# Kernel tuning notes

Hardware: AMD Instinct MI355X
Metric: run time of the kernel (lower is better)

## Reference

```python
import jax, jax.numpy as jnp
import numpy as np

EPS = 1e-08


def setup_inputs() -> dict:
    key = jax.random.key(0)
    k1, k2, k3 = jax.random.split(key, 3)
    N, IN_DIM, OUT_DIM = 8192, 512, 512
    h = jax.random.normal(k1, (N, IN_DIM), dtype=jnp.float32)
    adj = jax.random.randint(k2, (N, N), 0, 2, dtype=jnp.int32)
    # nn.Linear(in_dim, out_dim, bias=False) weight: [out_dim, in_dim]
    W = jax.random.normal(k3, (OUT_DIM, IN_DIM), dtype=jnp.float32) * (1.0 / np.sqrt(IN_DIM))
    return {"h": h, "adj": adj, "W": W}


def reference(h, adj, W):
    # Wh = h @ W^T  -> [N, out_dim]
    Wh = h @ W.T
    N = Wh.shape[0]
    norms = jnp.linalg.norm(Wh, axis=1, keepdims=True)  # [N, 1]
    # cosine similarity [N, N]
    sim = (Wh @ Wh.T) / (norms * norms.T + EPS)
    mask = (adj > 0) | jnp.eye(N, dtype=bool)
    sim_masked = jnp.where(mask, sim, -jnp.inf)
    alpha = jax.nn.softmax(sim_masked, axis=1)
    return alpha @ Wh
```

## Files before the change

### kernel.cpp

```cpp
#include <hip/hip_runtime.h>
#include <hip/hip_bf16.h>
#include <stdint.h>

#define NN 8192
#define DD 512

typedef unsigned short u16;
typedef unsigned long long u64;
typedef __attribute__((ext_vector_type(8))) short short8;
typedef __attribute__((ext_vector_type(4))) float f32x4;

__device__ __forceinline__ void gld_lds16(const void* g, void* l) {
  __builtin_amdgcn_global_load_lds(
      (const __attribute__((address_space(1))) uint32_t*)(uintptr_t)g,
      (__attribute__((address_space(3))) uint32_t*)(uintptr_t)l,
      16, 0, 0);
}

__device__ __forceinline__ u16 f2bf(float f) {
  __hip_bfloat16 b = __float2bfloat16(f);
  return __builtin_bit_cast(u16, b);
}

__global__ void fill_kernel(float* __restrict__ p, int n, float v) {
  int i = blockIdx.x * 256 + threadIdx.x;
  int stride = gridDim.x * 256;
  for (; i < n; i += stride) p[i] = v;
}

__global__ void cvt4_kernel(const float4* __restrict__ src, ushort4* __restrict__ dst, int n4) {
  int i = blockIdx.x * 256 + threadIdx.x;
  int stride = gridDim.x * 256;
  for (; i < n4; i += stride) {
    float4 v = src[i];
    ushort4 o;
    o.x = f2bf(v.x); o.y = f2bf(v.y); o.z = f2bf(v.z); o.w = f2bf(v.w);
    dst[i] = o;
  }
}

__global__ void pack_adj_kernel(const int* __restrict__ adj, u16* __restrict__ mask,
                                float* __restrict__ den) {
  const int row = blockIdx.x;
  const int t = threadIdx.x;
  if (t == 0) den[row] = 0.0f;
  const uint4* arow = (const uint4*)(adj + (size_t)row * NN);
  #pragma unroll
  for (int iter = 0; iter < 2; iter++) {
    const int c16 = iter * 256 + t;
    unsigned int bits = 0;
    #pragma unroll
    for (int g = 0; g < 4; g++) {
      uint4 v = arow[c16 * 4 + g];
      bits |= (v.x ? 1u : 0u) << (g * 4 + 0);
      bits |= (v.y ? 1u : 0u) << (g * 4 + 1);
      bits |= (v.z ? 1u : 0u) << (g * 4 + 2);
      bits |= (v.w ? 1u : 0u) << (g * 4 + 3);
    }
    mask[(size_t)row * (NN / 16) + c16] = (u16)bits;
  }
}

__global__ void rownorm_kernel(const float* __restrict__ Wh, float* __restrict__ invn) {
  int row = blockIdx.x;
  int l = threadIdx.x;
  const float4* p = (const float4*)(Wh + (size_t)row * DD);
  float4 a = p[l], b = p[l + 64];
  float s = a.x*a.x + a.y*a.y + a.z*a.z + a.w*a.w
          + b.x*b.x + b.y*b.y + b.z*b.z + b.w*b.w;
  #pragma unroll
  for (int off = 32; off; off >>= 1) s += __shfl_down(s, off);
  if (l == 0) invn[row] = 1.0f / sqrtf(s);
}

__global__ void u_wht_kernel(const float* __restrict__ Wh, const float* __restrict__ invn,
                             u16* __restrict__ U, u16* __restrict__ WhT) {
  __shared__ float tile[64][65];
  int i0 = blockIdx.x * 64, d0 = blockIdx.y * 64;
  int c = threadIdx.x & 63, rb = threadIdx.x >> 6;
  #pragma unroll
  for (int r = rb; r < 64; r += 4) {
    float v = Wh[(size_t)(i0 + r) * DD + d0 + c];
    tile[r][c] = v;
    U[(size_t)(i0 + r) * DD + d0 + c] = f2bf(v * invn[i0 + r]);
  }
  __syncthreads();
  #pragma unroll
  for (int r = rb; r < 64; r += 4) {
    WhT[(size_t)(d0 + r) * NN + i0 + c] = f2bf(tile[c][r]);
  }
}

__global__ void __launch_bounds__(256) gemm_wh(
    const u16* __restrict__ A, const u16* __restrict__ B,
    int Nn, int K, float* __restrict__ Cf)
{
  __shared__ __align__(16) u16 As[128 * 32];
  __shared__ __align__(16) u16 Bs[128 * 32];

  const int tid = threadIdx.x;
  const int w = tid >> 6;
  const int lane = tid & 63;
  const int lm = lane & 15;
  const int q = lane >> 4;
  const int row0 = blockIdx.y * 128;
  const int col0 = blockIdx.x * 128;
  const int RM = (w >> 1) * 64;
  const int RN = (w & 1) * 64;
  const int sr = tid >> 2;
  const int sk = (tid & 3) * 8;

  f32x4 acc[4][4];
  #pragma unroll
  for (int a_ = 0; a_ < 4; a_++)
    #pragma unroll
    for (int b_ = 0; b_ < 4; b_++)
      acc[a_][b_] = (f32x4){0.f, 0.f, 0.f, 0.f};

  const size_t Abase = (size_t)row0 * K;
  const size_t Bbase = (size_t)col0 * K;

  for (int k0 = 0; k0 < K; k0 += 32) {
    __syncthreads();
    gld_lds16(A + Abase + (size_t)sr * K + k0 + sk,        (char*)As + w * 1024);
    gld_lds16(A + Abase + (size_t)(sr + 64) * K + k0 + sk, (char*)As + 4096 + w * 1024);
    gld_lds16(B + Bbase + (size_t)sr * K + k0 + sk,        (char*)Bs + w * 1024);
    gld_lds16(B + Bbase + (size_t)(sr + 64) * K + k0 + sk, (char*)Bs + 4096 + w * 1024);
    __syncthreads();

    short8 af[4], bfr[4];
    #pragma unroll
    for (int mt = 0; mt < 4; mt++)
      af[mt] = *(const short8*)&As[(RM + mt * 16 + lm) * 32 + q * 8];
    #pragma unroll
    for (int nt = 0; nt < 4; nt++)
      bfr[nt] = *(const short8*)&Bs[(RN + nt * 16 + lm) * 32 + q * 8];

    #pragma unroll
    for (int mt = 0; mt < 4; mt++)
      #pragma unroll
      for (int nt = 0; nt < 4; nt++)
        acc[mt][nt] = __builtin_amdgcn_mfma_f32_16x16x32_bf16(af[mt], bfr[nt], acc[mt][nt], 0, 0, 0);
  }

  #pragma unroll
  for (int mt = 0; mt < 4; mt++) {
    const int ib = row0 + RM + mt * 16 + q * 4;
    #pragma unroll
    for (int rr = 0; rr < 4; rr++) {
      const int i = ib + rr;
      #pragma unroll
      for (int nt = 0; nt < 4; nt++) {
        const int jc = col0 + RN + nt * 16 + lm;
        Cf[(size_t)i * Nn + jc] = acc[mt][nt][rr];
      }
    }
  }
}

__global__ void __launch_bounds__(256) gemm_sim(
    const u16* __restrict__ U, const u64* __restrict__ maskw,
    u16* __restrict__ Pb, float* __restrict__ den)
{
  __shared__ __align__(16) u16 As[128 * 32];
  __shared__ __align__(16) u16 Bs[128 * 32];

  const int b = blockIdx.x;
  int bi = (int)((sqrtf(8.0f * (float)b + 1.0f) - 1.0f) * 0.5f);
  while ((bi + 1) * (bi + 2) / 2 <= b) bi++;
  while (bi * (bi + 1) / 2 > b) bi--;
  const int bj = b - bi * (bi + 1) / 2;

  const int tid = threadIdx.x;
  const int w = tid >> 6;
  const int lane = tid & 63;
  const int lm = lane & 15;
  const int q = lane >> 4;
  const int row0 = bi * 128;
  const int col0 = bj * 128;
  const int RM = (w >> 1) * 64;
  const int RN = (w & 1) * 64;
  const int sr = tid >> 2;
  const int sk = (tid & 3) * 8;
  const bool diag = (bi == bj);

  f32x4 acc[4][4];
  #pragma unroll
  for (int a_ = 0; a_ < 4; a_++)
    #pragma unroll
    for (int b_ = 0; b_ < 4; b_++)
      acc[a_][b_] = (f32x4){0.f, 0.f, 0.f, 0.f};

  const size_t Abase = (size_t)row0 * DD;
  const size_t Bbase = (size_t)col0 * DD;

  for (int k0 = 0; k0 < DD; k0 += 32) {
    __syncthreads();
    gld_lds16(U + Abase + (size_t)sr * DD + k0 + sk,        (char*)As + w * 1024);
    gld_lds16(U + Abase + (size_t)(sr + 64) * DD + k0 + sk, (char*)As + 4096 + w * 1024);
    gld_lds16(U + Bbase + (size_t)sr * DD + k0 + sk,        (char*)Bs + w * 1024);
    gld_lds16(U + Bbase + (size_t)(sr + 64) * DD + k0 + sk, (char*)Bs + 4096 + w * 1024);
    __syncthreads();

    short8 af[4], bfr[4];
    #pragma unroll
    for (int mt = 0; mt < 4; mt++)
      af[mt] = *(const short8*)&As[(RM + mt * 16 + lm) * 32 + q * 8];
    #pragma unroll
    for (int nt = 0; nt < 4; nt++)
      bfr[nt] = *(const short8*)&Bs[(RN + nt * 16 + lm) * 32 + q * 8];

    #pragma unroll
    for (int mt = 0; mt < 4; mt++)
      #pragma unroll
      for (int nt = 0; nt < 4; nt++)
        acc[mt][nt] = __builtin_amdgcn_mfma_f32_16x16x32_bf16(af[mt], bfr[nt], acc[mt][nt], 0, 0, 0);
  }

  const int wordIdx = (col0 + RN) >> 6;
  const int word2Idx = (row0 + RM) >> 6;

  u64 wrd2[4];
  if (!diag) {
    #pragma unroll
    for (int nt = 0; nt < 4; nt++) {
      const int jc = col0 + RN + nt * 16 + lm;
      wrd2[nt] = maskw[(size_t)jc * (NN / 64) + word2Idx];
    }
  }

  float msum[4] = {0.f, 0.f, 0.f, 0.f};

  #pragma unroll
  for (int mt = 0; mt < 4; mt++) {
    const int ib = row0 + RM + mt * 16 + q * 4;
    float pm[4][4];
    #pragma unroll
    for (int rr = 0; rr < 4; rr++) {
      const int i = ib + rr;
      const u64 wrd = maskw[(size_t)i * (NN / 64) + wordIdx];
      const int bit2 = mt * 16 + q * 4 + rr;
      float psum = 0.f;
      #pragma unroll
      for (int nt = 0; nt < 4; nt++) {
        const int jc = col0 + RN + nt * 16 + lm;
        const float ev = __expf(acc[mt][nt][rr]);
        const bool on = ((wrd >> (nt * 16 + lm)) & 1ull) || (diag && i == jc);
        const float p = on ? ev : 0.0f;
        psum += p;
        Pb[(size_t)i * NN + jc] = f2bf(p);
        if (!diag) {
          const bool on2 = (wrd2[nt] >> bit2) & 1ull;
          const float pmv = on2 ? ev : 0.0f;
          pm[nt][rr] = pmv;
          msum[nt] += pmv;
        }
      }
      #pragma unroll
      for (int off = 8; off; off >>= 1) psum += __shfl_down(psum, off, 16);
      if (lm == 0) atomicAdd(&den[i], psum);
    }
    if (!diag) {
      #pragma unroll
      for (int nt = 0; nt < 4; nt++) {
        const int jc = col0 + RN + nt * 16 + lm;
        ushort4 m4;
        m4.x = f2bf(pm[nt][0]); m4.y = f2bf(pm[nt][1]);
        m4.z = f2bf(pm[nt][2]); m4.w = f2bf(pm[nt][3]);
        *(ushort4*)&Pb[(size_t)jc * NN + ib] = m4;
      }
    }
  }

  if (!diag) {
    #pragma unroll
    for (int nt = 0; nt < 4; nt++) {
      float s = msum[nt];
      s += __shfl_xor(s, 16);
      s += __shfl_xor(s, 32);
      if (q == 0) atomicAdd(&den[col0 + RN + nt * 16 + lm], s);
    }
  }
}

__global__ void __launch_bounds__(512, 2) gemm_out(
    const u16* __restrict__ A,
    const u16* __restrict__ B,
    u16* __restrict__ part)
{
  __shared__ __align__(16) u16 As[128 * 32];
  __shared__ __align__(16) u16 Bs[512 * 32];

  const int tid = threadIdx.x;
  const int w = tid >> 6;
  const int lane = tid & 63;
  const int lm = lane & 15;
  const int q = lane >> 4;
  const int row0 = blockIdx.x * 128;
  const int z = blockIdx.y;
  const int RM = (w >> 2) * 64;
  const int RN = (w & 3) * 128;
  const int sr = tid >> 2;
  const int sk = (tid & 3) * 8;

  f32x4 acc[4][8];
  #pragma unroll
  for (int a_ = 0; a_ < 4; a_++)
    #pragma unroll
    for (int b_ = 0; b_ < 8; b_++)
      acc[a_][b_] = (f32x4){0.f, 0.f, 0.f, 0.f};

  const size_t Abase = (size_t)row0 * NN;
  const int kBegin = z * (NN / 8), kEnd = (z + 1) * (NN / 8);

  for (int k0 = kBegin; k0 < kEnd; k0 += 32) {
    __syncthreads();
    gld_lds16(A + Abase + (size_t)sr * NN + k0 + sk, (char*)As + w * 1024);
    #pragma unroll
    for (int c = 0; c < 4; c++)
      gld_lds16(B + (size_t)(c * 128 + sr) * NN + k0 + sk, (char*)Bs + c * 8192 + w * 1024);
    __syncthreads();

    short8 af[4], bfr[8];
    #pragma unroll
    for (int mt = 0; mt < 4; mt++)
      af[mt] = *(const short8*)&As[(RM + mt * 16 + lm) * 32 + q * 8];
    #pragma unroll
    for (int nt = 0; nt < 8; nt++)
      bfr[nt] = *(const short8*)&Bs[(RN + nt * 16 + lm) * 32 + q * 8];

    #pragma unroll
    for (int mt = 0; mt < 4; mt++)
      #pragma unroll
      for (int nt = 0; nt < 8; nt++)
        acc[mt][nt] = __builtin_amdgcn_mfma_f32_16x16x32_bf16(af[mt], bfr[nt], acc[mt][nt], 0, 0, 0);
  }

  u16* const pz = part + (size_t)z * NN * DD;
  #pragma unroll
  for (int mt = 0; mt < 4; mt++) {
    const int ib = row0 + RM + mt * 16 + q * 4;
    #pragma unroll
    for (int rr = 0; rr < 4; rr++) {
      const int i = ib + rr;
      #pragma unroll
      for (int nt = 0; nt < 8; nt++) {
        const int dc = RN + nt * 16 + lm;
        pz[(size_t)i * DD + dc] = f2bf(acc[mt][nt][rr]);
      }
    }
  }
}

__global__ void reduce8_kernel(const u16* __restrict__ part,
                               const float* __restrict__ den, float4* __restrict__ out) {
  const int idx = blockIdx.x * 256 + threadIdx.x;
  const int row = idx >> 6;
  const float dinv = 1.0f / den[row];
  float s[8] = {0, 0, 0, 0, 0, 0, 0, 0};
  #pragma unroll
  for (int zp = 0; zp < 8; zp++) {
    const uint4 u = ((const uint4*)(part + (size_t)zp * NN * DD))[idx];
    s[0] += __uint_as_float(u.x << 16); s[1] += __uint_as_float(u.x & 0xffff0000u);
    s[2] += __uint_as_float(u.y << 16); s[3] += __uint_as_float(u.y & 0xffff0000u);
    s[4] += __uint_as_float(u.z << 16); s[5] += __uint_as_float(u.z & 0xffff0000u);
    s[6] += __uint_as_float(u.w << 16); s[7] += __uint_as_float(u.w & 0xffff0000u);
  }
  float4 o0 = {s[0] * dinv, s[1] * dinv, s[2] * dinv, s[3] * dinv};
  float4 o1 = {s[4] * dinv, s[5] * dinv, s[6] * dinv, s[7] * dinv};
  out[idx * 2] = o0;
  out[idx * 2 + 1] = o1;
}

extern "C" void kernel_launch(void* const* d_in, const int* in_sizes, int n_in,
                              void* d_out, int out_size, void* d_ws, size_t ws_size,
                              hipStream_t stream) {
  const float* h = (const float*)d_in[0];
  const int* adj = (const int*)d_in[1];
  const float* W = (const float*)d_in[2];
  float* out = (float*)d_out;

  const size_t SZ_P    = (size_t)NN * NN * 2;
  const size_t SZ_MASK = (size_t)NN * NN / 8;
  const size_t SZ_WHT  = (size_t)DD * NN * 2;
  const size_t SZ_HB   = (size_t)NN * DD * 2;
  const size_t SZ_WB   = (size_t)DD * DD * 2;
  const size_t SZ_U    = (size_t)NN * DD * 2;
  const size_t SZ_WH   = (size_t)NN * DD * 4;
  const size_t SZ_PART = (size_t)8 * NN * DD * 2;
  const size_t NEEDED  = SZ_P + SZ_MASK + SZ_WHT + SZ_HB + SZ_WB + SZ_U + SZ_WH
                       + SZ_PART + 2 * (size_t)NN * 4;

  if (ws_size < NEEDED) {
    fill_kernel<<<256, 256, 0, stream>>>(out, out_size, 12345.0f);
    return;
  }

  char* ws = (char*)d_ws;
  size_t off = 0;
  u16*   P    = (u16*)(ws + off); off += SZ_P;
  u16*   mask = (u16*)(ws + off); off += SZ_MASK;
  u16*   WhT  = (u16*)(ws + off); off += SZ_WHT;
  u16*   hb   = (u16*)(ws + off); off += SZ_HB;
  u16*   Wb   = (u16*)(ws + off); off += SZ_WB;
  u16*   U    = (u16*)(ws + off); off += SZ_U;
  float* Wh   = (float*)(ws + off); off += SZ_WH;
  u16*   part = (u16*)(ws + off); off += SZ_PART;
  float* invn = (float*)(ws + off);
  float* den  = invn + NN;

  pack_adj_kernel<<<NN, 256, 0, stream>>>(adj, mask, den);
  cvt4_kernel<<<1024, 256, 0, stream>>>((const float4*)h, (ushort4*)hb, NN * DD / 4);
  cvt4_kernel<<<256, 256, 0, stream>>>((const float4*)W, (ushort4*)Wb, DD * DD / 4);
  gemm_wh<<<dim3(DD / 128, NN / 128), 256, 0, stream>>>(hb, Wb, DD, DD, Wh);
  rownorm_kernel<<<NN, 64, 0, stream>>>(Wh, invn);
  u_wht_kernel<<<dim3(NN / 64, DD / 64), 256, 0, stream>>>(Wh, invn, U, WhT);
  gemm_sim<<<64 * 65 / 2, 256, 0, stream>>>(U, (const u64*)mask, P, den);
  gemm_out<<<dim3(NN / 128, 8), 512, 0, stream>>>(P, WhT, part);
  reduce8_kernel<<<NN * DD / 8 / 256, 256, 0, stream>>>(part, den, (float4*)out);
}
```

Baseline: 655.2 us.

## Shrink gemm_out tile to 64 rows, use exp2 with prescaled norms

Each gemm_out block now covers 64 rows instead of 128, and each wave computes a 64x64 output slice. This halves the accumulator registers, which lets the launch bound ask for 4 blocks per CU and doubles the grid. The cost is that each loaded B tile is reused across fewer rows. In gemm_sim, exp is replaced by exp2f on inputs prescaled by sqrt(log2 e) folded into U. Probabilities are truncated to bf16 by bit masking rather than rounded, and the denominator sums the same truncated values so it stays consistent with P.

```diff
diff --git a/kernel.cpp b/kernel.cpp
--- a/kernel.cpp
+++ b/kernel.cpp
@@ -82,7 +82,7 @@
   for (int r = rb; r < 64; r += 4) {
     float v = Wh[(size_t)(i0 + r) * DD + d0 + c];
     tile[r][c] = v;
-    U[(size_t)(i0 + r) * DD + d0 + c] = f2bf(v * invn[i0 + r]);
+    U[(size_t)(i0 + r) * DD + d0 + c] = f2bf(v * (invn[i0 + r] * 1.2011224f));
   }
   __syncthreads();
   #pragma unroll
@@ -234,7 +234,7 @@
   #pragma unroll
   for (int mt = 0; mt < 4; mt++) {
     const int ib = row0 + RM + mt * 16 + q * 4;
-    float pm[4][4];
+    u16 pm[4][4];
     #pragma unroll
     for (int rr = 0; rr < 4; rr++) {
       const int i = ib + rr;
@@ -244,15 +244,16 @@
       #pragma unroll
       for (int nt = 0; nt < 4; nt++) {
         const int jc = col0 + RN + nt * 16 + lm;
-        const float ev = __expf(acc[mt][nt][rr]);
+        const float ev = exp2f(acc[mt][nt][rr]);
+        const float tv = __uint_as_float(__float_as_uint(ev) & 0xffff0000u);
         const bool on = ((wrd >> (nt * 16 + lm)) & 1ull) || (diag && i == jc);
-        const float p = on ? ev : 0.0f;
+        const float p = on ? tv : 0.0f;
         psum += p;
-        Pb[(size_t)i * NN + jc] = f2bf(p);
+        Pb[(size_t)i * NN + jc] = (u16)(__float_as_uint(p) >> 16);
         if (!diag) {
           const bool on2 = (wrd2[nt] >> bit2) & 1ull;
-          const float pmv = on2 ? ev : 0.0f;
-          pm[nt][rr] = pmv;
+          const float pmv = on2 ? tv : 0.0f;
+          pm[nt][rr] = (u16)(__float_as_uint(pmv) >> 16);
           msum[nt] += pmv;
         }
       }
@@ -265,8 +266,7 @@
       for (int nt = 0; nt < 4; nt++) {
         const int jc = col0 + RN + nt * 16 + lm;
         ushort4 m4;
-        m4.x = f2bf(pm[nt][0]); m4.y = f2bf(pm[nt][1]);
-        m4.z = f2bf(pm[nt][2]); m4.w = f2bf(pm[nt][3]);
+        m4.x = pm[nt][0]; m4.y = pm[nt][1]; m4.z = pm[nt][2]; m4.w = pm[nt][3];
         *(ushort4*)&Pb[(size_t)jc * NN + ib] = m4;
       }
     }
@@ -283,12 +283,12 @@
   }
 }
 
-__global__ void __launch_bounds__(512, 2) gemm_out(
+__global__ void __launch_bounds__(512, 4) gemm_out(
     const u16* __restrict__ A,
     const u16* __restrict__ B,
     u16* __restrict__ part)
 {
-  __shared__ __align__(16) u16 As[128 * 32];
+  __shared__ __align__(16) u16 As[64 * 32];
   __shared__ __align__(16) u16 Bs[512 * 32];
 
   const int tid = threadIdx.x;
@@ -296,56 +296,55 @@
   const int lane = tid & 63;
   const int lm = lane & 15;
   const int q = lane >> 4;
-  const int row0 = blockIdx.x * 128;
+  const int row0 = blockIdx.x * 64;
   const int z = blockIdx.y;
-  const int RM = (w >> 2) * 64;
-  const int RN = (w & 3) * 128;
-  const int sr = tid >> 2;
-  const int sk = (tid & 3) * 8;
-
-  f32x4 acc[4][8];
+  const int sr4 = lane >> 2;
+  const int sk = (lane & 3) * 8;
+
+  f32x4 acc[4][4];
   #pragma unroll
   for (int a_ = 0; a_ < 4; a_++)
     #pragma unroll
-    for (int b_ = 0; b_ < 8; b_++)
+    for (int b_ = 0; b_ < 4; b_++)
       acc[a_][b_] = (f32x4){0.f, 0.f, 0.f, 0.f};
 
-  const size_t Abase = (size_t)row0 * NN;
   const int kBegin = z * (NN / 8), kEnd = (z + 1) * (NN / 8);
 
   for (int k0 = kBegin; k0 < kEnd; k0 += 32) {
     __syncthreads();
-    gld_lds16(A + Abase + (size_t)sr * NN + k0 + sk, (char*)As + w * 1024);
+    if (w < 4)
+      gld_lds16(A + (size_t)(row0 + w * 16 + sr4) * NN + k0 + sk, (char*)As + w * 1024);
     #pragma unroll
     for (int c = 0; c < 4; c++)
-      gld_lds16(B + (size_t)(c * 128 + sr) * NN + k0 + sk, (char*)Bs + c * 8192 + w * 1024);
-    __syncthreads();
-
-    short8 af[4], bfr[8];
-    #pragma unroll
-    for (int mt = 0; mt < 4; mt++)
-      af[mt] = *(const short8*)&As[(RM + mt * 16 + lm) * 32 + q * 8];
-    #pragma unroll
-    for (int nt = 0; nt < 8; nt++)
-      bfr[nt] = *(const short8*)&Bs[(RN + nt * 16 + lm) * 32 + q * 8];
-
-    #pragma unroll
-    for (int mt = 0; mt < 4; mt++)
-      #pragma unroll
-      for (int nt = 0; nt < 8; nt++)
+      gld_lds16(B + (size_t)((w * 4 + c) * 16 + sr4) * NN + k0 + sk,
+                (char*)Bs + (w * 4 + c) * 1024);
+    __syncthreads();
+
+    short8 af[4], bfr[4];
+    #pragma unroll
+    for (int mt = 0; mt < 4; mt++)
+      af[mt] = *(const short8*)&As[(mt * 16 + lm) * 32 + q * 8];
+    #pragma unroll
+    for (int nt = 0; nt < 4; nt++)
+      bfr[nt] = *(const short8*)&Bs[(w * 64 + nt * 16 + lm) * 32 + q * 8];
+
+    #pragma unroll
+    for (int mt = 0; mt < 4; mt++)
+      #pragma unroll
+      for (int nt = 0; nt < 4; nt++)
         acc[mt][nt] = __builtin_amdgcn_mfma_f32_16x16x32_bf16(af[mt], bfr[nt], acc[mt][nt], 0, 0, 0);
   }
 
   u16* const pz = part + (size_t)z * NN * DD;
   #pragma unroll
   for (int mt = 0; mt < 4; mt++) {
-    const int ib = row0 + RM + mt * 16 + q * 4;
+    const int ib = row0 + mt * 16 + q * 4;
     #pragma unroll
     for (int rr = 0; rr < 4; rr++) {
       const int i = ib + rr;
       #pragma unroll
-      for (int nt = 0; nt < 8; nt++) {
-        const int dc = RN + nt * 16 + lm;
+      for (int nt = 0; nt < 4; nt++) {
+        const int dc = w * 64 + nt * 16 + lm;
         pz[(size_t)i * DD + dc] = f2bf(acc[mt][nt][rr]);
       }
     }
@@ -416,6 +415,6 @@
   rownorm_kernel<<<NN, 64, 0, stream>>>(Wh, invn);
   u_wht_kernel<<<dim3(NN / 64, DD / 64), 256, 0, stream>>>(Wh, invn, U, WhT);
   gemm_sim<<<64 * 65 / 2, 256, 0, stream>>>(U, (const u64*)mask, P, den);
-  gemm_out<<<dim3(NN / 128, 8), 512, 0, stream>>>(P, WhT, part);
+  gemm_out<<<dim3(NN / 64, 8), 512, 0, stream>>>(P, WhT, part);
   reduce8_kernel<<<NN * DD / 8 / 256, 256, 0, stream>>>(part, den, (float4*)out);
 }
```

Measured after the change: 659.6 us. No clear change (+0.7%).
